# Performance work log

Hardware: AMD Instinct MI355X
Metric: run time of the kernel (lower is better)

The kernel has to match this reference:

```python
import jax, jax.numpy as jnp
import numpy as np

B, H, I = 4096, 256, 32


def setup_inputs() -> dict:
    key = jax.random.key(0)
    k1, k2, k3, k4, k5 = jax.random.split(key, 5)
    idx = jax.random.randint(k1, (B,), 0, I)
    inp = jax.nn.one_hot(idx, I, dtype=jnp.float32)  # one-hot selector [B, I]
    hx = jax.random.normal(k2, (B, H), jnp.float32)
    weight_hh = jax.random.normal(k3, (3 * H, H, I), jnp.float32)
    bias_ih = jax.random.normal(k4, (3 * H, I), jnp.float32)
    bias_hh = jax.random.normal(k5, (3 * H, I), jnp.float32)
    return {"input": inp, "hx": hx, "weight_hh": weight_hh,
            "bias_ih": bias_ih, "bias_hh": bias_hh}


def reference(input, hx, weight_hh, bias_ih, bias_hh):
    # input is one-hot, so the broadcast-multiply-sum over the last axis is
    # mathematically a gather of the selected expert slice.
    idx = jnp.argmax(input, axis=-1)                      # [B]
    Wt = jnp.moveaxis(weight_hh, 2, 0)[idx]               # [B, 3H, H] selected recurrent weights
    rec = jnp.einsum('bgh,bh->bg', Wt, hx)                # [B, 3H]
    gates_i = bias_ih.T[idx]                              # [B, 3H]
    gates_h = rec + bias_hh.T[idx]                        # [B, 3H]
    ri, ui, ni = jnp.split(gates_i, 3, axis=1)
    rh, uh, nh = jnp.split(gates_h, 3, axis=1)
    reset_gate = jax.nn.sigmoid(ri + rh)
    update_gate = jax.nn.sigmoid(ui + uh)
    new_gate = jnp.tanh(ni + reset_gate * nh)
    hy = update_gate * hx + (1 - update_gate) * new_gate  # [B, H]
    return hy[None]
```

## Files before the change

kernel.cpp:

```cpp
#include <hip/hip_runtime.h>
#include <math.h>

#define B_N 4096
#define H_N 256
#define I_N 32
#define G3  768
#define NSEG 16
#define BKROW 4096

#define WS_SC      0
#define WS_BUCKET  2048
#define WS_B4      526336
#define WS_W5      657408
#define WS_NEEDED  13240320

typedef __attribute__((ext_vector_type(8))) _Float16 f16x8_t;
typedef __attribute__((ext_vector_type(4))) float f32x4_t;

__device__ __forceinline__ float sigm(float x) { return 1.0f / (1.0f + __expf(-x)); }
__device__ __forceinline__ float tanh_fast(float x) {
    float xc = fminf(fmaxf(x, -15.f), 15.f);
    float t = __expf(2.f * xc);
    return (t - 1.f) / (t + 1.f);
}

__global__ __launch_bounds__(256) void k_aux(
    const float* __restrict__ w, unsigned short* __restrict__ w5,
    const float* __restrict__ b_ih, const float* __restrict__ b_hh,
    float4* __restrict__ b4,
    const float* __restrict__ inp, int* __restrict__ sc,
    int* __restrict__ bucket)
{
    int bid = blockIdx.x;
    int t = threadIdx.x;
    if (bid < 768) {
        __shared__ float tl[8 * 1057];
        int r0 = (bid >> 3) * 8;
        int ks = bid & 7;
#pragma unroll
        for (int it = 0; it < 8; ++it) {
            int f4 = it * 256 + t;
            int e4 = (f4 & 7) * 4, hh = (f4 >> 3) & 31, r = f4 >> 8;
            float4 v = *(const float4*)(w + ((size_t)(r0 + r) * 256 + ks * 32 + hh) * 32 + e4);
            int bse = r * 1057 + hh * 33 + e4;
            tl[bse] = v.x; tl[bse + 1] = v.y; tl[bse + 2] = v.z; tl[bse + 3] = v.w;
        }
        __syncthreads();
        int rowgrp = r0 >> 4;
        int mbase = r0 & 15;
#pragma unroll
        for (int it = 0; it < 4; ++it) {
            int c = it * 256 + t;
            int m8 = c & 7, kg = (c >> 3) & 3, e = c >> 5;
            union { _Float16 h[8]; uint4 v; } hi;
#pragma unroll
            for (int t8 = 0; t8 < 8; ++t8) {
                float f = tl[m8 * 1057 + (kg * 8 + t8) * 33 + e];
                hi.h[t8] = (_Float16)f;
            }
            size_t chunk = ((size_t)(e * 8 + ks) * 48 + rowgrp) * 64 + kg * 16 + mbase + m8;
            ((uint4*)w5)[chunk] = hi.v;
        }
    } else if (bid < 800) {
        int bb = bid - 768;
        int e = t & 31;
        int tt = bb * 8 + (t >> 5);
        float r = b_ih[tt * 32 + e] + b_hh[tt * 32 + e];
        float u = b_ih[(256 + tt) * 32 + e] + b_hh[(256 + tt) * 32 + e];
        float ni = b_ih[(512 + tt) * 32 + e];
        float nh = b_hh[(512 + tt) * 32 + e];
        float4 o = {r, u, ni, nh};
        b4[e * 256 + tt] = o;
    } else {
        __shared__ int lhist[32];
        int seg = bid - 800;
        if (t < 32) lhist[t] = 0;
        __syncthreads();
        int b = seg * 256 + t;
        const float4* p = (const float4*)(inp + (size_t)b * I_N);
        int idx = 0;
#pragma unroll
        for (int k = 0; k < 8; ++k) {
            float4 v = p[k];
            if (v.x > 0.5f) idx = k * 4 + 0;
            if (v.y > 0.5f) idx = k * 4 + 1;
            if (v.z > 0.5f) idx = k * 4 + 2;
            if (v.w > 0.5f) idx = k * 4 + 3;
        }
        int lp = atomicAdd(&lhist[idx], 1);
        bucket[idx * BKROW + seg * 256 + lp] = b;
        __syncthreads();
        if (t < 32) sc[seg * 32 + t] = lhist[t];
    }
}

__global__ __launch_bounds__(256) void k_gemm_mfma(
    const unsigned short* __restrict__ w5,
    const float* __restrict__ hx, const float4* __restrict__ b4,
    const int* __restrict__ sc, const int* __restrict__ bucket,
    float* __restrict__ out)
{
    int bkt = blockIdx.x & 7, j0 = blockIdx.x >> 3;
    int t = threadIdx.x;

    int tot[4], nch[4];
#pragma unroll
    for (int i = 0; i < 4; ++i) {
        int e = bkt + 8 * i, s = 0;
#pragma unroll
        for (int j = 0; j < NSEG; ++j) s += sc[j * 32 + e];
        tot[i] = s; nch[i] = (s + 31) >> 5;
    }
    int c1 = nch[0], c2 = c1 + nch[1], c3 = c2 + nch[2], ntot = c3 + nch[3];

    __shared__ _Float16 Ah[32 * 256];
    __shared__ int bids[32];

    for (int jj = j0; jj < ntot; jj += 34) {
        int ei, ch;
        if (jj < c1)      { ei = 0; ch = jj; }
        else if (jj < c2) { ei = 1; ch = jj - c1; }
        else if (jj < c3) { ei = 2; ch = jj - c2; }
        else              { ei = 3; ch = jj - c3; }
        int e = bkt + 8 * ei;
        int M = tot[ei] - ch * 32; if (M > 32) M = 32;

        int row = t >> 3, c8 = t & 7;
        int b = -1;
        if (row < M) {
            int rank = ch * 32 + row;
            int acc = 0, seg = 0, off = 0;
#pragma unroll
            for (int j = 0; j < NSEG; ++j) {
                int c = sc[j * 32 + e];
                if (rank >= acc && rank < acc + c) { seg = j; off = rank - acc; }
                acc += c;
            }
            b = bucket[e * BKROW + seg * 256 + off];
        }
        if (c8 == 0) bids[row] = b;

        if (b >= 0) {
            const float* src = hx + ((size_t)b << 8) + c8 * 32;
            float fv[32];
#pragma unroll
            for (int p = 0; p < 8; ++p)
                *(float4*)&fv[p * 4] = *(const float4*)(src + p * 4);
#pragma unroll
            for (int p = 0; p < 4; ++p) {
                union { _Float16 h[8]; uint4 v; } hu;
#pragma unroll
                for (int jj2 = 0; jj2 < 8; ++jj2)
                    hu.h[jj2] = (_Float16)fv[p * 8 + jj2];
                int col = (c8 * 4 + p) ^ (row & 7);
                *(uint4*)&Ah[row * 256 + col * 8] = hu.v;
            }
        } else {
            uint4 z = {0, 0, 0, 0};
#pragma unroll
            for (int p = 0; p < 4; ++p) {
                int col = (c8 * 4 + p) ^ (row & 7);
                *(uint4*)&Ah[row * 256 + col * 8] = z;
            }
        }
        __syncthreads();

        int lane = t & 63, wv = t >> 6;
        int m16 = lane & 15, kg = lane >> 4;
        int q = blockIdx.y * 4 + wv;

        f32x4_t acc2[2][3];
#pragma unroll
        for (int tl2 = 0; tl2 < 2; ++tl2)
#pragma unroll
            for (int g = 0; g < 3; ++g) acc2[tl2][g] = (f32x4_t){0.f, 0.f, 0.f, 0.f};

        const unsigned short* b_p = w5 + ((size_t)(e * 8) * 48 + q) * 512 + (size_t)lane * 8;

#pragma unroll
        for (int ks = 0; ks < 8; ++ks) {
            int chs = ks * 4 + kg;
            int sw = (chs ^ (m16 & 7)) << 3;
            f16x8_t a_0 = *(const f16x8_t*)&Ah[m16 * 256 + sw];
            f16x8_t a_1 = *(const f16x8_t*)&Ah[(16 + m16) * 256 + sw];
#pragma unroll
            for (int g = 0; g < 3; ++g) {
                size_t foff = ((size_t)ks * 48 + g * 16) * 512;
                f16x8_t b_h = *(const f16x8_t*)(b_p + foff);
                acc2[0][g] = __builtin_amdgcn_mfma_f32_16x16x32_f16(a_0, b_h, acc2[0][g], 0, 0, 0);
                acc2[1][g] = __builtin_amdgcn_mfma_f32_16x16x32_f16(a_1, b_h, acc2[1][g], 0, 0, 0);
            }
        }

        int mg = (lane >> 4) * 4;
        int tt = q * 16 + m16;
        float4 bs = b4[e * 256 + tt];
#pragma unroll
        for (int tl2 = 0; tl2 < 2; ++tl2) {
#pragma unroll
            for (int i = 0; i < 4; ++i) {
                int mr = tl2 * 16 + mg + i;
                if (mr < M) {
                    int bb = bids[mr];
                    float x = hx[(size_t)bb * 256 + tt];
                    float r = sigm(acc2[tl2][0][i] + bs.x);
                    float u = sigm(acc2[tl2][1][i] + bs.y);
                    float n = tanh_fast(bs.z + r * (acc2[tl2][2][i] + bs.w));
                    out[(size_t)bb * 256 + tt] = u * x + (1.0f - u) * n;
                }
            }
        }
        __syncthreads();
    }
}

__global__ void k_naive(const float* __restrict__ inp, const float* __restrict__ hx,
                        const float* __restrict__ w, const float* __restrict__ b_ih,
                        const float* __restrict__ b_hh, float* __restrict__ out) {
    int b = blockIdx.x;
    int t = threadIdx.x;
    __shared__ float sx[H_N];
    __shared__ int sidx;
    if (t == 0) {
        int idx = 0;
        for (int i = 0; i < I_N; ++i)
            if (inp[b * I_N + i] > 0.5f) idx = i;
        sidx = idx;
    }
    sx[t] = hx[b * H_N + t];
    __syncthreads();
    int i = sidx;
    float a0 = 0.f, a1 = 0.f, a2 = 0.f;
    for (int h = 0; h < H_N; ++h) {
        float xv = sx[h];
        a0 = fmaf(w[(t * H_N + h) * I_N + i], xv, a0);
        a1 = fmaf(w[((256 + t) * H_N + h) * I_N + i], xv, a1);
        a2 = fmaf(w[((512 + t) * H_N + h) * I_N + i], xv, a2);
    }
    float r = sigm(b_ih[t * I_N + i] + a0 + b_hh[t * I_N + i]);
    float u = sigm(b_ih[(256 + t) * I_N + i] + a1 + b_hh[(256 + t) * I_N + i]);
    float n = tanhf(b_ih[(512 + t) * I_N + i] + r * (a2 + b_hh[(512 + t) * I_N + i]));
    out[b * H_N + t] = u * sx[t] + (1.0f - u) * n;
}

extern "C" void kernel_launch(void* const* d_in, const int* in_sizes, int n_in,
                              void* d_out, int out_size, void* d_ws, size_t ws_size,
                              hipStream_t stream) {
    const float* inp  = (const float*)d_in[0];
    const float* hx   = (const float*)d_in[1];
    const float* w    = (const float*)d_in[2];
    const float* b_ih = (const float*)d_in[3];
    const float* b_hh = (const float*)d_in[4];
    float* out = (float*)d_out;

    if (ws_size < (size_t)WS_NEEDED) {
        k_naive<<<B_N, H_N, 0, stream>>>(inp, hx, w, b_ih, b_hh, out);
        return;
    }

    char* ws = (char*)d_ws;
    int* sc     = (int*)(ws + WS_SC);
    int* bucket = (int*)(ws + WS_BUCKET);
    float4* b4  = (float4*)(ws + WS_B4);
    unsigned short* w5 = (unsigned short*)(ws + WS_W5);

    k_aux<<<816, 256, 0, stream>>>(w, w5, b_ih, b_hh, b4, inp, sc, bucket);
    k_gemm_mfma<<<dim3(272, 4), 256, 0, stream>>>(w5, hx, b4, sc, bucket, out);
}
```

Baseline: 28.22 us.

## Shrink MFMA row tile to 16, prefetch weight fragments, reuse staged hx

Each expert bucket is now split into chunks of 16 rows instead of 32. Each wave runs one row of MFMAs per gate instead of two. This roughly doubles the number of chunks, so more of the grid-strided blocks have work, at the cost of reading each expert's weight slice more often. The weight fragments for the next k-step are now loaded one iteration ahead (software prefetch). The epilogue reads hx from the fp16 copy staged in LDS instead of reloading fp32 from global memory, which slightly lowers precision in the final blend. A register/occupancy hint is also added via launch_bounds(256, 4).

```diff
diff --git a/kernel.cpp b/kernel.cpp
--- a/kernel.cpp
+++ b/kernel.cpp
@@ -94,7 +94,7 @@
     }
 }
 
-__global__ __launch_bounds__(256) void k_gemm_mfma(
+__global__ __launch_bounds__(256, 4) void k_gemm_mfma(
     const unsigned short* __restrict__ w5,
     const float* __restrict__ hx, const float4* __restrict__ b4,
     const int* __restrict__ sc, const int* __restrict__ bucket,
@@ -103,32 +103,42 @@
     int bkt = blockIdx.x & 7, j0 = blockIdx.x >> 3;
     int t = threadIdx.x;
 
-    int tot[4], nch[4];
-#pragma unroll
-    for (int i = 0; i < 4; ++i) {
-        int e = bkt + 8 * i, s = 0;
-#pragma unroll
-        for (int j = 0; j < NSEG; ++j) s += sc[j * 32 + e];
-        tot[i] = s; nch[i] = (s + 31) >> 5;
-    }
-    int c1 = nch[0], c2 = c1 + nch[1], c3 = c2 + nch[2], ntot = c3 + nch[3];
-
-    __shared__ _Float16 Ah[32 * 256];
-    __shared__ int bids[32];
+    int tot0 = 0, tot1 = 0, tot2 = 0, tot3 = 0;
+#pragma unroll
+    for (int j = 0; j < NSEG; ++j) {
+        tot0 += sc[j * 32 + bkt];
+        tot1 += sc[j * 32 + bkt + 8];
+        tot2 += sc[j * 32 + bkt + 16];
+        tot3 += sc[j * 32 + bkt + 24];
+    }
+    int c1 = (tot0 + 15) >> 4;
+    int c2 = c1 + ((tot1 + 15) >> 4);
+    int c3 = c2 + ((tot2 + 15) >> 4);
+    int ntot = c3 + ((tot3 + 15) >> 4);
+
+    __shared__ _Float16 Ah[16 * 256];
+    __shared__ int bids[16];
+
+    int lane = t & 63, wv = t >> 6;
+    int m16 = lane & 15, kg = lane >> 4;
+    int q = blockIdx.y * 4 + wv;
 
     for (int jj = j0; jj < ntot; jj += 34) {
-        int ei, ch;
-        if (jj < c1)      { ei = 0; ch = jj; }
-        else if (jj < c2) { ei = 1; ch = jj - c1; }
-        else if (jj < c3) { ei = 2; ch = jj - c2; }
-        else              { ei = 3; ch = jj - c3; }
+        int ei = (jj < c1) ? 0 : (jj < c2) ? 1 : (jj < c3) ? 2 : 3;
+        int ch = (jj < c1) ? jj : (jj < c2) ? jj - c1 : (jj < c3) ? jj - c2 : jj - c3;
+        int te = (jj < c1) ? tot0 : (jj < c2) ? tot1 : (jj < c3) ? tot2 : tot3;
         int e = bkt + 8 * ei;
-        int M = tot[ei] - ch * 32; if (M > 32) M = 32;
-
-        int row = t >> 3, c8 = t & 7;
+        int M = te - ch * 16; if (M > 16) M = 16;
+
+        const unsigned short* b_p = w5 + ((size_t)(e * 8) * 48 + q) * 512 + (size_t)lane * 8;
+        f16x8_t bc0 = *(const f16x8_t*)(b_p);
+        f16x8_t bc1 = *(const f16x8_t*)(b_p + (size_t)16 * 512);
+        f16x8_t bc2 = *(const f16x8_t*)(b_p + (size_t)32 * 512);
+
+        int row = t >> 4, c16 = t & 15;
         int b = -1;
         if (row < M) {
-            int rank = ch * 32 + row;
+            int rank = ch * 16 + row;
             int acc = 0, seg = 0, off = 0;
 #pragma unroll
             for (int j = 0; j < NSEG; ++j) {
@@ -138,76 +148,68 @@
             }
             b = bucket[e * BKROW + seg * 256 + off];
         }
-        if (c8 == 0) bids[row] = b;
+        if (c16 == 0) bids[row] = b;
 
         if (b >= 0) {
-            const float* src = hx + ((size_t)b << 8) + c8 * 32;
-            float fv[32];
-#pragma unroll
-            for (int p = 0; p < 8; ++p)
+            const float* src = hx + ((size_t)b << 8) + c16 * 16;
+            float fv[16];
+#pragma unroll
+            for (int p = 0; p < 4; ++p)
                 *(float4*)&fv[p * 4] = *(const float4*)(src + p * 4);
 #pragma unroll
-            for (int p = 0; p < 4; ++p) {
+            for (int p = 0; p < 2; ++p) {
                 union { _Float16 h[8]; uint4 v; } hu;
 #pragma unroll
                 for (int jj2 = 0; jj2 < 8; ++jj2)
                     hu.h[jj2] = (_Float16)fv[p * 8 + jj2];
-                int col = (c8 * 4 + p) ^ (row & 7);
+                int col = (c16 * 2 + p) ^ (row & 7);
                 *(uint4*)&Ah[row * 256 + col * 8] = hu.v;
             }
         } else {
             uint4 z = {0, 0, 0, 0};
 #pragma unroll
-            for (int p = 0; p < 4; ++p) {
-                int col = (c8 * 4 + p) ^ (row & 7);
+            for (int p = 0; p < 2; ++p) {
+                int col = (c16 * 2 + p) ^ (row & 7);
                 *(uint4*)&Ah[row * 256 + col * 8] = z;
             }
         }
         __syncthreads();
 
-        int lane = t & 63, wv = t >> 6;
-        int m16 = lane & 15, kg = lane >> 4;
-        int q = blockIdx.y * 4 + wv;
-
-        f32x4_t acc2[2][3];
-#pragma unroll
-        for (int tl2 = 0; tl2 < 2; ++tl2)
-#pragma unroll
-            for (int g = 0; g < 3; ++g) acc2[tl2][g] = (f32x4_t){0.f, 0.f, 0.f, 0.f};
-
-        const unsigned short* b_p = w5 + ((size_t)(e * 8) * 48 + q) * 512 + (size_t)lane * 8;
+        f32x4_t ac0 = {0.f, 0.f, 0.f, 0.f};
+        f32x4_t ac1 = {0.f, 0.f, 0.f, 0.f};
+        f32x4_t ac2 = {0.f, 0.f, 0.f, 0.f};
 
 #pragma unroll
         for (int ks = 0; ks < 8; ++ks) {
-            int chs = ks * 4 + kg;
-            int sw = (chs ^ (m16 & 7)) << 3;
-            f16x8_t a_0 = *(const f16x8_t*)&Ah[m16 * 256 + sw];
-            f16x8_t a_1 = *(const f16x8_t*)&Ah[(16 + m16) * 256 + sw];
-#pragma unroll
-            for (int g = 0; g < 3; ++g) {
-                size_t foff = ((size_t)ks * 48 + g * 16) * 512;
-                f16x8_t b_h = *(const f16x8_t*)(b_p + foff);
-                acc2[0][g] = __builtin_amdgcn_mfma_f32_16x16x32_f16(a_0, b_h, acc2[0][g], 0, 0, 0);
-                acc2[1][g] = __builtin_amdgcn_mfma_f32_16x16x32_f16(a_1, b_h, acc2[1][g], 0, 0, 0);
-            }
+            f16x8_t bn0 = bc0, bn1 = bc1, bn2 = bc2;
+            if (ks < 7) {
+                const unsigned short* np = b_p + (size_t)(ks + 1) * 48 * 512;
+                bn0 = *(const f16x8_t*)(np);
+                bn1 = *(const f16x8_t*)(np + (size_t)16 * 512);
+                bn2 = *(const f16x8_t*)(np + (size_t)32 * 512);
+            }
+            int sw = ((ks * 4 + kg) ^ (m16 & 7)) << 3;
+            f16x8_t a0 = *(const f16x8_t*)&Ah[m16 * 256 + sw];
+            ac0 = __builtin_amdgcn_mfma_f32_16x16x32_f16(a0, bc0, ac0, 0, 0, 0);
+            ac1 = __builtin_amdgcn_mfma_f32_16x16x32_f16(a0, bc1, ac1, 0, 0, 0);
+            ac2 = __builtin_amdgcn_mfma_f32_16x16x32_f16(a0, bc2, ac2, 0, 0, 0);
+            bc0 = bn0; bc1 = bn1; bc2 = bn2;
         }
 
         int mg = (lane >> 4) * 4;
         int tt = q * 16 + m16;
         float4 bs = b4[e * 256 + tt];
 #pragma unroll
-        for (int tl2 = 0; tl2 < 2; ++tl2) {
-#pragma unroll
-            for (int i = 0; i < 4; ++i) {
-                int mr = tl2 * 16 + mg + i;
-                if (mr < M) {
-                    int bb = bids[mr];
-                    float x = hx[(size_t)bb * 256 + tt];
-                    float r = sigm(acc2[tl2][0][i] + bs.x);
-                    float u = sigm(acc2[tl2][1][i] + bs.y);
-                    float n = tanh_fast(bs.z + r * (acc2[tl2][2][i] + bs.w));
-                    out[(size_t)bb * 256 + tt] = u * x + (1.0f - u) * n;
-                }
+        for (int i = 0; i < 4; ++i) {
+            int mr = mg + i;
+            if (mr < M) {
+                int bb = bids[mr];
+                int xc = ((tt >> 3) ^ (mr & 7)) * 8 + (tt & 7);
+                float x = (float)Ah[mr * 256 + xc];
+                float r = sigm(ac0[i] + bs.x);
+                float u = sigm(ac1[i] + bs.y);
+                float n = tanh_fast(bs.z + r * (ac2[i] + bs.w));
+                out[(size_t)bb * 256 + tt] = u * x + (1.0f - u) * n;
             }
         }
         __syncthreads();
```

Measured after the change: 27.16 us, median of 3. -3.7%, faster.
